# Kernel tuning notes

Measured on AMD Instinct MI355X. Metric: run time of the kernel, lower is better.

The kernel has to match this reference:

```python
import jax, jax.numpy as jnp
import numpy as np

IN, OUT = 8192, 8192


def setup_inputs() -> dict:
    key = jax.random.key(0)
    k1, k2, k3, k4 = jax.random.split(key, 4)
    base = jax.random.normal(k1, (1, IN), dtype=jnp.float32)
    width = jax.random.uniform(k2, (1, IN), dtype=jnp.float32)  # >= 0
    l = base - width  # lower bound
    u = base + width  # upper bound, l <= u
    weight = jax.random.normal(k3, (IN, OUT), dtype=jnp.float32) * 0.02
    bias = jax.random.normal(k4, (OUT,), dtype=jnp.float32) * 0.02
    return {"l": l, "u": u, "weight": weight, "bias": bias}


def reference(l, u, weight, bias):
    # Interval bound propagation through y = x @ W + b, W: [in, out].
    # mask = 1 where W >= 0 (sign==+1), 0 where W < 0, 0.5 where W == 0
    mask = (1.0 + jnp.sign(weight)) * 0.5  # [in, out]
    lb = l.T  # [in, 1], broadcasts against [in, out] (same math as .repeat)
    ub = u.T  # [in, 1]
    mask_l = lb * mask + ub * (1.0 - mask)  # pick l for W>=0, u for W<0
    bound_l = jnp.sum(mask_l * weight, axis=0) + bias  # [out]
    mask_u = ub * mask + lb * (1.0 - mask)  # pick u for W>=0, l for W<0
    bound_u = jnp.sum(mask_u * weight, axis=0) + bias  # [out]
    return (bound_l[None, :], bound_u[None, :])
```

## Files before the change

### kernel.cpp

```cpp
#include <hip/hip_runtime.h>

#define IN_DIM  8192
#define OUT_DIM 8192
#define TPB 256
#define COLS_PER_BLOCK (TPB * 4)
#define ROWS_PER_BLOCK 32

__global__ void __launch_bounds__(TPB) init_out_kernel(const float* __restrict__ bias,
                                                       float* __restrict__ out) {
    int j = blockIdx.x * TPB + threadIdx.x;
    float b = bias[j];
    out[j] = b;
    out[OUT_DIM + j] = b;
}

__global__ void __launch_bounds__(TPB) ibp_kernel(const float* __restrict__ l,
                                                  const float* __restrict__ u,
                                                  const float* __restrict__ W,
                                                  float* __restrict__ out) {
    __shared__ float sc[ROWS_PER_BLOCK];
    __shared__ float sr[ROWS_PER_BLOCK];

    const int t    = threadIdx.x;
    const int col0 = blockIdx.x * COLS_PER_BLOCK + t * 4;
    const int row0 = blockIdx.y * ROWS_PER_BLOCK;

    if (t < ROWS_PER_BLOCK) {
        float lv = l[row0 + t];
        float uv = u[row0 + t];
        sc[t] = 0.5f * (lv + uv);
        sr[t] = 0.5f * (uv - lv);
    }
    __syncthreads();

    float cwx = 0.f, cwy = 0.f, cwz = 0.f, cww = 0.f;
    float rax = 0.f, ray = 0.f, raz = 0.f, raw = 0.f;

    const float4* Wp = reinterpret_cast<const float4*>(
        W + (size_t)row0 * OUT_DIM + col0);

    #pragma unroll 8
    for (int i = 0; i < ROWS_PER_BLOCK; ++i) {
        float4 w = Wp[(size_t)i * (OUT_DIM / 4)];
        float c = sc[i];
        float r = sr[i];
        cwx = fmaf(c, w.x, cwx);  rax = fmaf(r, fabsf(w.x), rax);
        cwy = fmaf(c, w.y, cwy);  ray = fmaf(r, fabsf(w.y), ray);
        cwz = fmaf(c, w.z, cwz);  raz = fmaf(r, fabsf(w.z), raz);
        cww = fmaf(c, w.w, cww);  raw = fmaf(r, fabsf(w.w), raw);
    }

    atomicAdd(&out[col0 + 0], cwx - rax);
    atomicAdd(&out[col0 + 1], cwy - ray);
    atomicAdd(&out[col0 + 2], cwz - raz);
    atomicAdd(&out[col0 + 3], cww - raw);
    atomicAdd(&out[OUT_DIM + col0 + 0], cwx + rax);
    atomicAdd(&out[OUT_DIM + col0 + 1], cwy + ray);
    atomicAdd(&out[OUT_DIM + col0 + 2], cwz + raz);
    atomicAdd(&out[OUT_DIM + col0 + 3], cww + raw);
}

extern "C" void kernel_launch(void* const* d_in, const int* in_sizes, int n_in,
                              void* d_out, int out_size, void* d_ws, size_t ws_size,
                              hipStream_t stream) {
    const float* l    = (const float*)d_in[0];
    const float* u    = (const float*)d_in[1];
    const float* W    = (const float*)d_in[2];
    const float* bias = (const float*)d_in[3];
    float* out = (float*)d_out;

    init_out_kernel<<<OUT_DIM / TPB, TPB, 0, stream>>>(bias, out);

    dim3 grid(OUT_DIM / COLS_PER_BLOCK, IN_DIM / ROWS_PER_BLOCK);
    ibp_kernel<<<grid, TPB, 0, stream>>>(l, u, W, out);
}
```

Measured before the change: 375.4 us.

## Replace global atomics with workspace partials and a separate reduction kernel

```diff
diff --git a/kernel.cpp b/kernel.cpp
--- a/kernel.cpp
+++ b/kernel.cpp
@@ -5,19 +5,12 @@
 #define TPB 256
 #define COLS_PER_BLOCK (TPB * 4)
 #define ROWS_PER_BLOCK 32
+#define NCHUNK (IN_DIM / ROWS_PER_BLOCK)
 
-__global__ void __launch_bounds__(TPB) init_out_kernel(const float* __restrict__ bias,
-                                                       float* __restrict__ out) {
-    int j = blockIdx.x * TPB + threadIdx.x;
-    float b = bias[j];
-    out[j] = b;
-    out[OUT_DIM + j] = b;
-}
-
-__global__ void __launch_bounds__(TPB) ibp_kernel(const float* __restrict__ l,
-                                                  const float* __restrict__ u,
-                                                  const float* __restrict__ W,
-                                                  float* __restrict__ out) {
+__global__ void __launch_bounds__(TPB) ibp_partial_kernel(const float* __restrict__ l,
+                                                          const float* __restrict__ u,
+                                                          const float* __restrict__ W,
+                                                          float* __restrict__ ws) {
     __shared__ float sc[ROWS_PER_BLOCK];
     __shared__ float sr[ROWS_PER_BLOCK];
 
@@ -50,14 +43,31 @@
         cww = fmaf(c, w.w, cww);  raw = fmaf(r, fabsf(w.w), raw);
     }
 
-    atomicAdd(&out[col0 + 0], cwx - rax);
-    atomicAdd(&out[col0 + 1], cwy - ray);
-    atomicAdd(&out[col0 + 2], cwz - raz);
-    atomicAdd(&out[col0 + 3], cww - raw);
-    atomicAdd(&out[OUT_DIM + col0 + 0], cwx + rax);
-    atomicAdd(&out[OUT_DIM + col0 + 1], cwy + ray);
-    atomicAdd(&out[OUT_DIM + col0 + 2], cwz + raz);
-    atomicAdd(&out[OUT_DIM + col0 + 3], cww + raw);
+    float4 pl = make_float4(cwx - rax, cwy - ray, cwz - raz, cww - raw);
+    float4 pu = make_float4(cwx + rax, cwy + ray, cwz + raz, cww + raw);
+
+    float4* wsl = reinterpret_cast<float4*>(
+        ws + (size_t)blockIdx.y * OUT_DIM + col0);
+    float4* wsu = reinterpret_cast<float4*>(
+        ws + (size_t)NCHUNK * OUT_DIM + (size_t)blockIdx.y * OUT_DIM + col0);
+    *wsl = pl;
+    *wsu = pu;
+}
+
+__global__ void __launch_bounds__(TPB) ibp_reduce_kernel(const float* __restrict__ ws,
+                                                         const float* __restrict__ bias,
+                                                         float* __restrict__ out) {
+    const int t = blockIdx.x * TPB + threadIdx.x;
+    const int b = t >> 13;
+    const int j = t & (OUT_DIM - 1);
+
+    const float* p = ws + (size_t)b * NCHUNK * OUT_DIM + j;
+    float s = 0.f;
+    #pragma unroll 8
+    for (int c = 0; c < NCHUNK; ++c)
+        s += p[(size_t)c * OUT_DIM];
+
+    out[t] = s + bias[j];
 }
 
 extern "C" void kernel_launch(void* const* d_in, const int* in_sizes, int n_in,
@@ -68,9 +78,10 @@
     const float* W    = (const float*)d_in[2];
     const float* bias = (const float*)d_in[3];
     float* out = (float*)d_out;
+    float* ws  = (float*)d_ws;
 
-    init_out_kernel<<<OUT_DIM / TPB, TPB, 0, stream>>>(bias, out);
+    dim3 grid1(OUT_DIM / COLS_PER_BLOCK, NCHUNK);
+    ibp_partial_kernel<<<grid1, TPB, 0, stream>>>(l, u, W, ws);
 
-    dim3 grid(OUT_DIM / COLS_PER_BLOCK, IN_DIM / ROWS_PER_BLOCK);
-    ibp_kernel<<<grid, TPB, 0, stream>>>(l, u, W, out);
+    ibp_reduce_kernel<<<(2 * OUT_DIM) / TPB, TPB, 0, stream>>>(ws, bias, out);
 }
```

Result: no change. 371.5 us (-1.0%).
